# Kernel optimization log

Hardware: AMD Instinct MI355X
Metric: run time of the kernel (lower is better)

## Reference

```python
import jax, jax.numpy as jnp
import numpy as np

N_NODES = 100000
N_EDGES = 1600000
HIDDEN = 64
NUM_GRAPHS = 512


def setup_inputs() -> dict:
    key = jax.random.key(0)
    k1, k2, k3, k4, k5, k6 = jax.random.split(key, 6)
    x = jax.random.normal(k1, (N_NODES, HIDDEN), dtype=jnp.float32)
    edge_index = jax.random.randint(k2, (2, N_EDGES), 0, N_NODES, dtype=jnp.int64)
    batch = jnp.sort(jax.random.randint(k3, (N_NODES,), 0, NUM_GRAPHS, dtype=jnp.int64))
    # SAGPooling's internal GraphConv(64 -> 1): lin_rel (with bias) on aggregated
    # neighbor features, lin_root (no bias) on self features.
    s = 1.0 / np.sqrt(HIDDEN)
    W_rel = jax.random.uniform(k4, (HIDDEN, 1), dtype=jnp.float32, minval=-s, maxval=s)
    b_rel = jax.random.uniform(k5, (1,), dtype=jnp.float32, minval=-s, maxval=s)
    W_root = jax.random.uniform(k6, (HIDDEN, 1), dtype=jnp.float32, minval=-s, maxval=s)
    return {"x": x, "edge_index": edge_index, "batch": batch,
            "W_rel": W_rel, "b_rel": b_rel, "W_root": W_root}


def reference(x, edge_index, batch, W_rel, b_rel, W_root):
    n = x.shape[0]
    src, dst = edge_index[0], edge_index[1]
    # GraphConv (aggr='add'): sum x_j over in-edges, then lin_rel(aggr)+lin_root(x)
    aggr = jax.ops.segment_sum(x[src], dst, num_segments=n)          # [N, H]
    score = (aggr @ W_rel + b_rel + x @ W_root)[:, 0]                # [N]
    # min_score=-1 -> scores softmax-normalized per graph; all nodes kept in order
    m = jax.ops.segment_max(score, batch, num_segments=NUM_GRAPHS)   # [G]
    e = jnp.exp(score - m[batch])
    z = jax.ops.segment_sum(e, batch, num_segments=NUM_GRAPHS)       # [G]
    att = e / z[batch]                                               # [N]
    att_x = x * att[:, None]                                         # [N, H]
    # global_add_pool
    return jax.ops.segment_sum(att_x, batch, num_segments=NUM_GRAPHS)  # [G, H]
```

## Files before the change

### kernel.cpp

```cpp
#include <hip/hip_runtime.h>
#include <math.h>
#include <stdint.h>


#define H 64
#define TILE 4096
#define NTHR_S 1024
#define EPT (TILE / NTHR_S)
#define BUCKET_SZ 256
#define MAX_NB 400
#define NREP 8
#define SUBCAP 768
#define CAP (NREP * SUBCAP)
#define PSCALE 16384.0f
#define INV_PSCALE 6.103515625e-05f

__global__ __launch_bounds__(256) void node_prep(
    const float4* __restrict__ x4, const float4* __restrict__ W_rel4,
    const float4* __restrict__ W_root4,
    float* __restrict__ p, float* __restrict__ r,
    float* __restrict__ num, float* __restrict__ z,
    unsigned int* __restrict__ cursor,
    int n_nodes, int num_elems, int n_graphs, int nb)
{
    int gid = (int)(blockIdx.x * blockDim.x + threadIdx.x);
    if (gid < num_elems) num[gid] = 0.0f;
    else if (gid < num_elems + n_graphs) z[gid - num_elems] = 0.0f;
    else if (gid < num_elems + n_graphs + nb * NREP) {
        int idx = gid - num_elems - n_graphs;
        int rep = idx / nb;
        int k   = idx - rep * nb;
        cursor[idx] = (unsigned int)(k * CAP + rep * SUBCAP);
    }

    int node = blockIdx.x * 64 + (threadIdx.x >> 2);
    int q    = threadIdx.x & 3;
    if (node >= n_nodes) return;

    float pv = 0.0f, rv = 0.0f;
    #pragma unroll
    for (int kk = 0; kk < 4; ++kk) {
        float4 v  = x4[node * 16 + kk * 4 + q];
        float4 wr = W_rel4[kk * 4 + q];
        float4 wo = W_root4[kk * 4 + q];
        pv += v.x * wr.x + v.y * wr.y + v.z * wr.z + v.w * wr.w;
        rv += v.x * wo.x + v.y * wo.y + v.z * wo.z + v.w * wo.w;
    }
    pv += __shfl_xor(pv, 1, 64); pv += __shfl_xor(pv, 2, 64);
    rv += __shfl_xor(rv, 1, 64); rv += __shfl_xor(rv, 2, 64);
    if (q == 0) { p[node] = pv; r[node] = rv; }
}

__global__ __launch_bounds__(NTHR_S) void edge_sort(
    const int* __restrict__ src, const int* __restrict__ dst,
    const float* __restrict__ p,
    unsigned int* __restrict__ cursor, unsigned int* __restrict__ sorted_g,
    int n_edges, int nb)
{
    __shared__ unsigned int hist[MAX_NB];
    __shared__ unsigned int offs[MAX_NB];
    __shared__ unsigned int gbase[MAX_NB];
    __shared__ unsigned int wtot[8];
    __shared__ unsigned int svals[TILE];
    __shared__ unsigned short sbid[TILE];

    int b = blockIdx.x;
    int rep = b & (NREP - 1);
    int base = b * TILE;
    int tile_n = min(TILE, n_edges - base);
    int tid = threadIdx.x;

    if (tid < nb) hist[tid] = 0;
    __syncthreads();

    unsigned int dd[EPT]; int ss[EPT];
    float pv[EPT];
    unsigned int bk[EPT], pk[EPT], slot[EPT];

    int j0 = tid * EPT;
    if (j0 + EPT <= tile_n) {
        int4 s4 = *(const int4*)(src + base + j0);
        int4 d4 = *(const int4*)(dst + base + j0);
        ss[0] = s4.x; ss[1] = s4.y; ss[2] = s4.z; ss[3] = s4.w;
        dd[0] = (unsigned int)d4.x; dd[1] = (unsigned int)d4.y;
        dd[2] = (unsigned int)d4.z; dd[3] = (unsigned int)d4.w;
    } else {
        #pragma unroll
        for (int u = 0; u < EPT; ++u) {
            int j = j0 + u;
            if (j < tile_n) { ss[u] = src[base + j];
                              dd[u] = (unsigned int)dst[base + j]; }
            else dd[u] = 0xFFFFFFFFu;
        }
    }
    #pragma unroll
    for (int u = 0; u < EPT; ++u)
        if (dd[u] != 0xFFFFFFFFu) pv[u] = p[ss[u]];
    #pragma unroll
    for (int u = 0; u < EPT; ++u) {
        if (dd[u] != 0xFFFFFFFFu) {
            bk[u] = dd[u] >> 8;
            int q = (int)__float2int_rn(pv[u] * PSCALE);
            q = max(-8388607, min(8388607, q));
            pk[u] = ((unsigned int)q << 8) | (dd[u] & 255u);
            slot[u] = atomicAdd(&hist[bk[u]], 1u);
        }
    }
    __syncthreads();

    int wv = tid >> 6, ln = tid & 63;
    unsigned int v = 0, xs = 0;
    if (wv < 7) {
        int bin = wv * 64 + ln;
        v = (bin < nb) ? hist[bin] : 0;
        xs = v;
        #pragma unroll
        for (int off = 1; off < 64; off <<= 1) {
            unsigned int y = __shfl_up(xs, off, 64);
            if (ln >= off) xs += y;
        }
        if (ln == 63) wtot[wv] = xs;
    }
    __syncthreads();
    if (wv < 7) {
        int bin = wv * 64 + ln;
        unsigned int pre = 0;
        #pragma unroll
        for (int w2 = 0; w2 < 7; ++w2)
            pre += (w2 < wv) ? wtot[w2] : 0u;
        if (bin < nb) {
            offs[bin]  = pre + xs - v;
            gbase[bin] = v ? atomicAdd(&cursor[rep * nb + bin], v) : 0u;
        }
    }
    __syncthreads();

    #pragma unroll
    for (int u = 0; u < EPT; ++u) {
        if (dd[u] != 0xFFFFFFFFu) {
            unsigned int pos = offs[bk[u]] + slot[u];
            svals[pos] = pk[u];
            sbid[pos]  = (unsigned short)bk[u];
        }
    }
    __syncthreads();

    for (int j = tid; j < tile_n; j += NTHR_S) {
        unsigned int bb = sbid[j];
        unsigned int gi = gbase[bb] + ((unsigned int)j - offs[bb]);
        unsigned int lim = bb * (unsigned int)CAP
                         + (unsigned int)(rep + 1) * SUBCAP;
        if (gi < lim)
            sorted_g[gi] = svals[j];
    }
}

__global__ __launch_bounds__(512) void bucket_pool(
    const unsigned int* __restrict__ sorted_g,
    const unsigned int* __restrict__ cursor,
    const float* __restrict__ r,
    const float* __restrict__ x,
    const int* __restrict__ batch,
    float* __restrict__ num, float* __restrict__ z,
    int n_nodes, int nb)
{
    __shared__ int acc[BUCKET_SZ];
    __shared__ float e_lds[BUCKET_SZ];
    __shared__ int g_lds[BUCKET_SZ];
    __shared__ unsigned int cnts[NREP];
    __shared__ float pnum[2 * NREP][H];
    __shared__ float pz[2 * NREP];
    __shared__ int   sgid[2 * NREP];

    int k = blockIdx.x;
    int tid = threadIdx.x;
    int node0 = k * BUCKET_SZ;

    if (tid < BUCKET_SZ) acc[tid] = 0;
    else {
        int t2 = tid - BUCKET_SZ;
        int node = node0 + t2;
        g_lds[t2] = (node < n_nodes) ? batch[node] : -1;
    }
    if (tid < NREP) {
        unsigned int begr = (unsigned int)(k * CAP + tid * SUBCAP);
        cnts[tid] = min(cursor[tid * nb + k] - begr, (unsigned int)SUBCAP);
    }
    if (tid < 2 * NREP) sgid[tid] = -1;
    __syncthreads();

    {
        int wv = tid >> 6, ln = tid & 63;
        unsigned int beg = (unsigned int)(k * CAP + wv * SUBCAP);
        unsigned int cnt = cnts[wv];
        unsigned int n4  = cnt & ~3u;
        for (unsigned int j = ln * 4; j < n4; j += 256) {
            uint4 v = *(const uint4*)(sorted_g + beg + j);
            atomicAdd(&acc[v.x & 255u], (int)v.x >> 8);
            atomicAdd(&acc[v.y & 255u], (int)v.y >> 8);
            atomicAdd(&acc[v.z & 255u], (int)v.z >> 8);
            atomicAdd(&acc[v.w & 255u], (int)v.w >> 8);
        }
        for (unsigned int j = n4 + ln; j < cnt; j += 64) {
            unsigned int v = sorted_g[beg + j];
            atomicAdd(&acc[v & 255u], (int)v >> 8);
        }
    }
    __syncthreads();

    if (tid < BUCKET_SZ) {
        int node = node0 + tid;
        e_lds[tid] = (node < n_nodes)
                   ? __expf((float)acc[tid] * INV_PSCALE + r[node]) : 0.0f;
    }
    __syncthreads();

    int wid = tid >> 6, lane = tid & 63;
    int l0 = wid * 32;
    int row0 = node0 + l0;
    int s0 = wid * 2;
    if (row0 < n_nodes) {
        int rend = min(row0 + 32, n_nodes);
        int gF = g_lds[l0];
        int gL = g_lds[rend - 1 - node0];
        float sA = 0.0f, sB = 0.0f, zA = 0.0f, zB = 0.0f;

        if (rend - row0 == 32) {
            float xv[32];
            const float* xp = x + (size_t)row0 * H + lane;
            #pragma unroll
            for (int u = 0; u < 32; ++u)
                xv[u] = xp[u * H];
            #pragma unroll
            for (int u = 0; u < 32; ++u) {
                int li = l0 + u;
                int g = g_lds[li];
                float e = e_lds[li];
                float v = xv[u] * e;
                if (g == gF)      { sA += v; zA += e; }
                else if (g == gL) { sB += v; zB += e; }
                else {
                    unsafeAtomicAdd(&num[g * H + lane], v);
                    if (lane == 0) unsafeAtomicAdd(&z[g], e);
                }
            }
        } else {
            for (int i = row0; i < rend; ++i) {
                int li = i - node0;
                int g = g_lds[li];
                float e = e_lds[li];
                float v = x[(size_t)i * H + lane] * e;
                if (g == gF)      { sA += v; zA += e; }
                else if (g == gL) { sB += v; zB += e; }
                else {
                    unsafeAtomicAdd(&num[g * H + lane], v);
                    if (lane == 0) unsafeAtomicAdd(&z[g], e);
                }
            }
        }
        pnum[s0][lane] = sA;
        if (lane == 0) { sgid[s0] = gF; pz[s0] = zA; }
        if (gL != gF) {
            pnum[s0 + 1][lane] = sB;
            if (lane == 0) { sgid[s0 + 1] = gL; pz[s0 + 1] = zB; }
        }
    }
    __syncthreads();

    if (wid == 0) {
        float run = 0.0f, runz = 0.0f; int cur = -1;
        for (int s = 0; s < 2 * NREP; ++s) {
            int id = sgid[s];
            if (id < 0) continue;
            float v  = pnum[s][lane];
            float zv = pz[s];
            if (id != cur) {
                if (cur >= 0) {
                    unsafeAtomicAdd(&num[cur * H + lane], run);
                    if (lane == 0) unsafeAtomicAdd(&z[cur], runz);
                }
                cur = id; run = v; runz = zv;
            } else { run += v; runz += zv; }
        }
        if (cur >= 0) {
            unsafeAtomicAdd(&num[cur * H + lane], run);
            if (lane == 0) unsafeAtomicAdd(&z[cur], runz);
        }
    }
}

__global__ __launch_bounds__(256) void finalize(
    const float* __restrict__ num, const float* __restrict__ z,
    float* __restrict__ out, int num_elems)
{
    int i = (int)(blockIdx.x * blockDim.x + threadIdx.x);
    if (i >= num_elems) return;
    float zz = z[i >> 6];
    out[i] = (zz != 0.0f) ? num[i] / zz : 0.0f;
}

extern "C" void kernel_launch(void* const* d_in, const int* in_sizes, int n_in,
                              void* d_out, int out_size, void* d_ws, size_t ws_size,
                              hipStream_t stream)
{
    const float* x      = (const float*)d_in[0];
    const int*   eidx   = (const int*)d_in[1];
    const int*   batch  = (const int*)d_in[2];
    const float* W_rel  = (const float*)d_in[3];
    const float* W_root = (const float*)d_in[5];
    float* out = (float*)d_out;

    const int n_nodes  = in_sizes[0] / H;
    const int n_edges  = in_sizes[1] / 2;
    const int n_graphs = out_size / H;
    const int nb     = (n_nodes + BUCKET_SZ - 1) / BUCKET_SZ;
    const int ntiles = (n_edges + TILE - 1) / TILE;

    const int* src = eidx;
    const int* dst = eidx + n_edges;

    float* p     = (float*)d_ws;
    float* r     = p + n_nodes;
    float* z     = r + n_nodes;
    float* num   = z + n_graphs;
    unsigned int* cursor = (unsigned int*)(num + out_size);
    uintptr_t raw = (uintptr_t)(cursor + nb * NREP);
    unsigned int* sorted_g = (unsigned int*)((raw + 15) & ~(uintptr_t)15);

    int np_blocks = (n_nodes + 63) / 64;
    node_prep<<<np_blocks, 256, 0, stream>>>(
        (const float4*)x, (const float4*)W_rel, (const float4*)W_root,
        p, r, num, z, cursor, n_nodes, out_size, n_graphs, nb);
    edge_sort<<<ntiles, NTHR_S, 0, stream>>>(src, dst, p, cursor, sorted_g,
                                             n_edges, nb);
    bucket_pool<<<nb, 512, 0, stream>>>(sorted_g, cursor, r, x, batch,
                                        num, z, n_nodes, nb);
    finalize<<<(out_size + 255) / 256, 256, 0, stream>>>(num, z, out, out_size);
}
```

Before: 110.5 us.

## Fuse four kernels into one persistent cooperative kernel with grid syncs

Replaces the node_prep, edge_sort, bucket_pool and finalize launches with a single cooperative kernel of 256 blocks of 1024 threads, using grid.sync between phases. Each phase grid-strides over its work (nodes, edge tiles, buckets), which removes three kernel launch gaps. The bucket phase is reshaped for 1024 threads: two waves per replica, 16 rows per wave and 32 segments. The cost is grid-wide barriers, lower occupancy from the large LDS footprint and fixed block count, and ~391 edge tiles over 256 blocks causing load imbalance.

```diff
diff --git a/kernel.cpp b/kernel.cpp
--- a/kernel.cpp
+++ b/kernel.cpp
@@ -1,12 +1,13 @@
 #include <hip/hip_runtime.h>
+#include <hip/hip_cooperative_groups.h>
 #include <math.h>
 #include <stdint.h>
 
+namespace cg = cooperative_groups;
+
 
 #define H 64
 #define TILE 4096
-#define NTHR_S 1024
-#define EPT (TILE / NTHR_S)
 #define BUCKET_SZ 256
 #define MAX_NB 400
 #define NREP 8
@@ -14,289 +15,284 @@
 #define CAP (NREP * SUBCAP)
 #define PSCALE 16384.0f
 #define INV_PSCALE 6.103515625e-05f
-
-__global__ __launch_bounds__(256) void node_prep(
+#define NBLK 256
+#define NTHR 1024
+#define EPT (TILE / NTHR)
+#define NSEG 32
+
+__global__ __launch_bounds__(NTHR) void fused_pipeline(
     const float4* __restrict__ x4, const float4* __restrict__ W_rel4,
     const float4* __restrict__ W_root4,
+    const int* __restrict__ src, const int* __restrict__ dst,
+    const int* __restrict__ batch,
     float* __restrict__ p, float* __restrict__ r,
-    float* __restrict__ num, float* __restrict__ z,
-    unsigned int* __restrict__ cursor,
-    int n_nodes, int num_elems, int n_graphs, int nb)
+    float* __restrict__ z, float* __restrict__ num,
+    unsigned int* __restrict__ cursor, unsigned int* __restrict__ sorted_g,
+    float* __restrict__ out,
+    int n_nodes, int n_edges, int n_graphs, int nb, int ntiles, int out_size)
 {
-    int gid = (int)(blockIdx.x * blockDim.x + threadIdx.x);
-    if (gid < num_elems) num[gid] = 0.0f;
-    else if (gid < num_elems + n_graphs) z[gid - num_elems] = 0.0f;
-    else if (gid < num_elems + n_graphs + nb * NREP) {
-        int idx = gid - num_elems - n_graphs;
-        int rep = idx / nb;
-        int k   = idx - rep * nb;
-        cursor[idx] = (unsigned int)(k * CAP + rep * SUBCAP);
-    }
-
-    int node = blockIdx.x * 64 + (threadIdx.x >> 2);
-    int q    = threadIdx.x & 3;
-    if (node >= n_nodes) return;
-
-    float pv = 0.0f, rv = 0.0f;
-    #pragma unroll
-    for (int kk = 0; kk < 4; ++kk) {
-        float4 v  = x4[node * 16 + kk * 4 + q];
-        float4 wr = W_rel4[kk * 4 + q];
-        float4 wo = W_root4[kk * 4 + q];
-        pv += v.x * wr.x + v.y * wr.y + v.z * wr.z + v.w * wr.w;
-        rv += v.x * wo.x + v.y * wo.y + v.z * wo.z + v.w * wo.w;
-    }
-    pv += __shfl_xor(pv, 1, 64); pv += __shfl_xor(pv, 2, 64);
-    rv += __shfl_xor(rv, 1, 64); rv += __shfl_xor(rv, 2, 64);
-    if (q == 0) { p[node] = pv; r[node] = rv; }
-}
-
-__global__ __launch_bounds__(NTHR_S) void edge_sort(
-    const int* __restrict__ src, const int* __restrict__ dst,
-    const float* __restrict__ p,
-    unsigned int* __restrict__ cursor, unsigned int* __restrict__ sorted_g,
-    int n_edges, int nb)
-{
+    cg::grid_group grid = cg::this_grid();
+
     __shared__ unsigned int hist[MAX_NB];
     __shared__ unsigned int offs[MAX_NB];
     __shared__ unsigned int gbase[MAX_NB];
     __shared__ unsigned int wtot[8];
     __shared__ unsigned int svals[TILE];
     __shared__ unsigned short sbid[TILE];
-
-    int b = blockIdx.x;
-    int rep = b & (NREP - 1);
-    int base = b * TILE;
-    int tile_n = min(TILE, n_edges - base);
-    int tid = threadIdx.x;
-
-    if (tid < nb) hist[tid] = 0;
-    __syncthreads();
-
-    unsigned int dd[EPT]; int ss[EPT];
-    float pv[EPT];
-    unsigned int bk[EPT], pk[EPT], slot[EPT];
-
-    int j0 = tid * EPT;
-    if (j0 + EPT <= tile_n) {
-        int4 s4 = *(const int4*)(src + base + j0);
-        int4 d4 = *(const int4*)(dst + base + j0);
-        ss[0] = s4.x; ss[1] = s4.y; ss[2] = s4.z; ss[3] = s4.w;
-        dd[0] = (unsigned int)d4.x; dd[1] = (unsigned int)d4.y;
-        dd[2] = (unsigned int)d4.z; dd[3] = (unsigned int)d4.w;
-    } else {
-        #pragma unroll
-        for (int u = 0; u < EPT; ++u) {
-            int j = j0 + u;
-            if (j < tile_n) { ss[u] = src[base + j];
-                              dd[u] = (unsigned int)dst[base + j]; }
-            else dd[u] = 0xFFFFFFFFu;
-        }
-    }
-    #pragma unroll
-    for (int u = 0; u < EPT; ++u)
-        if (dd[u] != 0xFFFFFFFFu) pv[u] = p[ss[u]];
-    #pragma unroll
-    for (int u = 0; u < EPT; ++u) {
-        if (dd[u] != 0xFFFFFFFFu) {
-            bk[u] = dd[u] >> 8;
-            int q = (int)__float2int_rn(pv[u] * PSCALE);
-            q = max(-8388607, min(8388607, q));
-            pk[u] = ((unsigned int)q << 8) | (dd[u] & 255u);
-            slot[u] = atomicAdd(&hist[bk[u]], 1u);
-        }
-    }
-    __syncthreads();
-
-    int wv = tid >> 6, ln = tid & 63;
-    unsigned int v = 0, xs = 0;
-    if (wv < 7) {
-        int bin = wv * 64 + ln;
-        v = (bin < nb) ? hist[bin] : 0;
-        xs = v;
-        #pragma unroll
-        for (int off = 1; off < 64; off <<= 1) {
-            unsigned int y = __shfl_up(xs, off, 64);
-            if (ln >= off) xs += y;
-        }
-        if (ln == 63) wtot[wv] = xs;
-    }
-    __syncthreads();
-    if (wv < 7) {
-        int bin = wv * 64 + ln;
-        unsigned int pre = 0;
-        #pragma unroll
-        for (int w2 = 0; w2 < 7; ++w2)
-            pre += (w2 < wv) ? wtot[w2] : 0u;
-        if (bin < nb) {
-            offs[bin]  = pre + xs - v;
-            gbase[bin] = v ? atomicAdd(&cursor[rep * nb + bin], v) : 0u;
-        }
-    }
-    __syncthreads();
-
-    #pragma unroll
-    for (int u = 0; u < EPT; ++u) {
-        if (dd[u] != 0xFFFFFFFFu) {
-            unsigned int pos = offs[bk[u]] + slot[u];
-            svals[pos] = pk[u];
-            sbid[pos]  = (unsigned short)bk[u];
-        }
-    }
-    __syncthreads();
-
-    for (int j = tid; j < tile_n; j += NTHR_S) {
-        unsigned int bb = sbid[j];
-        unsigned int gi = gbase[bb] + ((unsigned int)j - offs[bb]);
-        unsigned int lim = bb * (unsigned int)CAP
-                         + (unsigned int)(rep + 1) * SUBCAP;
-        if (gi < lim)
-            sorted_g[gi] = svals[j];
-    }
-}
-
-__global__ __launch_bounds__(512) void bucket_pool(
-    const unsigned int* __restrict__ sorted_g,
-    const unsigned int* __restrict__ cursor,
-    const float* __restrict__ r,
-    const float* __restrict__ x,
-    const int* __restrict__ batch,
-    float* __restrict__ num, float* __restrict__ z,
-    int n_nodes, int nb)
-{
     __shared__ int acc[BUCKET_SZ];
     __shared__ float e_lds[BUCKET_SZ];
     __shared__ int g_lds[BUCKET_SZ];
     __shared__ unsigned int cnts[NREP];
-    __shared__ float pnum[2 * NREP][H];
-    __shared__ float pz[2 * NREP];
-    __shared__ int   sgid[2 * NREP];
-
-    int k = blockIdx.x;
-    int tid = threadIdx.x;
-    int node0 = k * BUCKET_SZ;
-
-    if (tid < BUCKET_SZ) acc[tid] = 0;
-    else {
-        int t2 = tid - BUCKET_SZ;
-        int node = node0 + t2;
-        g_lds[t2] = (node < n_nodes) ? batch[node] : -1;
-    }
-    if (tid < NREP) {
-        unsigned int begr = (unsigned int)(k * CAP + tid * SUBCAP);
-        cnts[tid] = min(cursor[tid * nb + k] - begr, (unsigned int)SUBCAP);
-    }
-    if (tid < 2 * NREP) sgid[tid] = -1;
-    __syncthreads();
+    __shared__ float pnum[NSEG][H];
+    __shared__ float pz[NSEG];
+    __shared__ int   sgid[NSEG];
+
+    int tid = threadIdx.x, bid = blockIdx.x;
+    int gt  = bid * NTHR + tid;
+    int wid = tid >> 6, lane = tid & 63;
+
+    if (gt < out_size) num[gt] = 0.0f;
+    else if (gt < out_size + n_graphs) z[gt - out_size] = 0.0f;
+    else if (gt < out_size + n_graphs + nb * NREP) {
+        int idx = gt - out_size - n_graphs;
+        int rep = idx / nb;
+        int k   = idx - rep * nb;
+        cursor[idx] = (unsigned int)(k * CAP + rep * SUBCAP);
+    }
 
     {
-        int wv = tid >> 6, ln = tid & 63;
-        unsigned int beg = (unsigned int)(k * CAP + wv * SUBCAP);
-        unsigned int cnt = cnts[wv];
-        unsigned int n4  = cnt & ~3u;
-        for (unsigned int j = ln * 4; j < n4; j += 256) {
-            uint4 v = *(const uint4*)(sorted_g + beg + j);
-            atomicAdd(&acc[v.x & 255u], (int)v.x >> 8);
-            atomicAdd(&acc[v.y & 255u], (int)v.y >> 8);
-            atomicAdd(&acc[v.z & 255u], (int)v.z >> 8);
-            atomicAdd(&acc[v.w & 255u], (int)v.w >> 8);
-        }
-        for (unsigned int j = n4 + ln; j < cnt; j += 64) {
-            unsigned int v = sorted_g[beg + j];
-            atomicAdd(&acc[v & 255u], (int)v >> 8);
-        }
-    }
-    __syncthreads();
-
-    if (tid < BUCKET_SZ) {
-        int node = node0 + tid;
-        e_lds[tid] = (node < n_nodes)
-                   ? __expf((float)acc[tid] * INV_PSCALE + r[node]) : 0.0f;
-    }
-    __syncthreads();
-
-    int wid = tid >> 6, lane = tid & 63;
-    int l0 = wid * 32;
-    int row0 = node0 + l0;
-    int s0 = wid * 2;
-    if (row0 < n_nodes) {
-        int rend = min(row0 + 32, n_nodes);
-        int gF = g_lds[l0];
-        int gL = g_lds[rend - 1 - node0];
-        float sA = 0.0f, sB = 0.0f, zA = 0.0f, zB = 0.0f;
-
-        if (rend - row0 == 32) {
-            float xv[32];
-            const float* xp = x + (size_t)row0 * H + lane;
+        int q = gt & 3;
+        for (int node = (gt >> 2); node < n_nodes; node += (NBLK * NTHR) / 4) {
+            float pv = 0.0f, rv = 0.0f;
             #pragma unroll
-            for (int u = 0; u < 32; ++u)
-                xv[u] = xp[u * H];
+            for (int kk = 0; kk < 4; ++kk) {
+                float4 v  = x4[node * 16 + kk * 4 + q];
+                float4 wr = W_rel4[kk * 4 + q];
+                float4 wo = W_root4[kk * 4 + q];
+                pv += v.x * wr.x + v.y * wr.y + v.z * wr.z + v.w * wr.w;
+                rv += v.x * wo.x + v.y * wo.y + v.z * wo.z + v.w * wo.w;
+            }
+            pv += __shfl_xor(pv, 1, 64); pv += __shfl_xor(pv, 2, 64);
+            rv += __shfl_xor(rv, 1, 64); rv += __shfl_xor(rv, 2, 64);
+            if (q == 0) { p[node] = pv; r[node] = rv; }
+        }
+    }
+    grid.sync();
+
+    for (int t = bid; t < ntiles; t += NBLK) {
+        int rep = t & (NREP - 1);
+        int base = t * TILE;
+        int tile_n = min(TILE, n_edges - base);
+
+        if (tid < nb) hist[tid] = 0;
+        __syncthreads();
+
+        unsigned int dd[EPT]; int ss[EPT];
+        float pv[EPT];
+        unsigned int bk[EPT], pk[EPT], slot[EPT];
+
+        int j0 = tid * EPT;
+        if (j0 + EPT <= tile_n) {
+            int4 s4 = *(const int4*)(src + base + j0);
+            int4 d4 = *(const int4*)(dst + base + j0);
+            ss[0] = s4.x; ss[1] = s4.y; ss[2] = s4.z; ss[3] = s4.w;
+            dd[0] = (unsigned int)d4.x; dd[1] = (unsigned int)d4.y;
+            dd[2] = (unsigned int)d4.z; dd[3] = (unsigned int)d4.w;
+        } else {
             #pragma unroll
-            for (int u = 0; u < 32; ++u) {
-                int li = l0 + u;
-                int g = g_lds[li];
-                float e = e_lds[li];
-                float v = xv[u] * e;
-                if (g == gF)      { sA += v; zA += e; }
-                else if (g == gL) { sB += v; zB += e; }
-                else {
-                    unsafeAtomicAdd(&num[g * H + lane], v);
-                    if (lane == 0) unsafeAtomicAdd(&z[g], e);
+            for (int u = 0; u < EPT; ++u) {
+                int j = j0 + u;
+                if (j < tile_n) { ss[u] = src[base + j];
+                                  dd[u] = (unsigned int)dst[base + j]; }
+                else dd[u] = 0xFFFFFFFFu;
+            }
+        }
+        #pragma unroll
+        for (int u = 0; u < EPT; ++u)
+            if (dd[u] != 0xFFFFFFFFu) pv[u] = p[ss[u]];
+        #pragma unroll
+        for (int u = 0; u < EPT; ++u) {
+            if (dd[u] != 0xFFFFFFFFu) {
+                bk[u] = dd[u] >> 8;
+                int qv = (int)__float2int_rn(pv[u] * PSCALE);
+                qv = max(-8388607, min(8388607, qv));
+                pk[u] = ((unsigned int)qv << 8) | (dd[u] & 255u);
+                slot[u] = atomicAdd(&hist[bk[u]], 1u);
+            }
+        }
+        __syncthreads();
+
+        unsigned int v = 0, xs = 0;
+        if (wid < 7) {
+            int bin = wid * 64 + lane;
+            v = (bin < nb) ? hist[bin] : 0;
+            xs = v;
+            #pragma unroll
+            for (int off = 1; off < 64; off <<= 1) {
+                unsigned int y = __shfl_up(xs, off, 64);
+                if (lane >= off) xs += y;
+            }
+            if (lane == 63) wtot[wid] = xs;
+        }
+        __syncthreads();
+        if (wid < 7) {
+            int bin = wid * 64 + lane;
+            unsigned int pre = 0;
+            #pragma unroll
+            for (int w2 = 0; w2 < 7; ++w2)
+                pre += (w2 < wid) ? wtot[w2] : 0u;
+            if (bin < nb) {
+                offs[bin]  = pre + xs - v;
+                gbase[bin] = v ? atomicAdd(&cursor[rep * nb + bin], v) : 0u;
+            }
+        }
+        __syncthreads();
+
+        #pragma unroll
+        for (int u = 0; u < EPT; ++u) {
+            if (dd[u] != 0xFFFFFFFFu) {
+                unsigned int pos = offs[bk[u]] + slot[u];
+                svals[pos] = pk[u];
+                sbid[pos]  = (unsigned short)bk[u];
+            }
+        }
+        __syncthreads();
+
+        for (int j = tid; j < tile_n; j += NTHR) {
+            unsigned int bb = sbid[j];
+            unsigned int gi = gbase[bb] + ((unsigned int)j - offs[bb]);
+            unsigned int lim = bb * (unsigned int)CAP
+                             + (unsigned int)(rep + 1) * SUBCAP;
+            if (gi < lim)
+                sorted_g[gi] = svals[j];
+        }
+        __syncthreads();
+    }
+    grid.sync();
+
+    const float* x = (const float*)x4;
+    for (int k = bid; k < nb; k += NBLK) {
+        __syncthreads();
+        int node0 = k * BUCKET_SZ;
+
+        if (tid < BUCKET_SZ) acc[tid] = 0;
+        else if (tid < 2 * BUCKET_SZ) {
+            int t2 = tid - BUCKET_SZ;
+            int node = node0 + t2;
+            g_lds[t2] = (node < n_nodes) ? batch[node] : -1;
+        }
+        if (tid < NREP) {
+            unsigned int begr = (unsigned int)(k * CAP + tid * SUBCAP);
+            cnts[tid] = min(cursor[tid * nb + k] - begr, (unsigned int)SUBCAP);
+        }
+        if (tid < NSEG) sgid[tid] = -1;
+        __syncthreads();
+
+        {
+            int rep_id = wid >> 1;
+            int sub    = ((wid & 1) << 6) + lane;
+            unsigned int beg = (unsigned int)(k * CAP + rep_id * SUBCAP);
+            unsigned int cnt = cnts[rep_id];
+            unsigned int n4  = cnt & ~3u;
+            for (unsigned int j = (unsigned int)sub * 4; j < n4; j += 512) {
+                uint4 vv = *(const uint4*)(sorted_g + beg + j);
+                atomicAdd(&acc[vv.x & 255u], (int)vv.x >> 8);
+                atomicAdd(&acc[vv.y & 255u], (int)vv.y >> 8);
+                atomicAdd(&acc[vv.z & 255u], (int)vv.z >> 8);
+                atomicAdd(&acc[vv.w & 255u], (int)vv.w >> 8);
+            }
+            for (unsigned int j = n4 + (unsigned int)sub; j < cnt; j += 128) {
+                unsigned int vv = sorted_g[beg + j];
+                atomicAdd(&acc[vv & 255u], (int)vv >> 8);
+            }
+        }
+        __syncthreads();
+
+        if (tid < BUCKET_SZ) {
+            int node = node0 + tid;
+            e_lds[tid] = (node < n_nodes)
+                       ? __expf((float)acc[tid] * INV_PSCALE + r[node]) : 0.0f;
+        }
+        __syncthreads();
+
+        int l0 = wid * 16;
+        int row0 = node0 + l0;
+        int s0 = wid * 2;
+        if (row0 < n_nodes) {
+            int rend = min(row0 + 16, n_nodes);
+            int gF = g_lds[l0];
+            int gL = g_lds[rend - 1 - node0];
+            float sA = 0.0f, sB = 0.0f, zA = 0.0f, zB = 0.0f;
+
+            if (rend - row0 == 16) {
+                float xv[16];
+                const float* xp = x + (size_t)row0 * H + lane;
+                #pragma unroll
+                for (int u = 0; u < 16; ++u)
+                    xv[u] = xp[u * H];
+                #pragma unroll
+                for (int u = 0; u < 16; ++u) {
+                    int li = l0 + u;
+                    int g = g_lds[li];
+                    float e = e_lds[li];
+                    float vv = xv[u] * e;
+                    if (g == gF)      { sA += vv; zA += e; }
+                    else if (g == gL) { sB += vv; zB += e; }
+                    else {
+                        unsafeAtomicAdd(&num[g * H + lane], vv);
+                        if (lane == 0) unsafeAtomicAdd(&z[g], e);
+                    }
                 }
-            }
-        } else {
-            for (int i = row0; i < rend; ++i) {
-                int li = i - node0;
-                int g = g_lds[li];
-                float e = e_lds[li];
-                float v = x[(size_t)i * H + lane] * e;
-                if (g == gF)      { sA += v; zA += e; }
-                else if (g == gL) { sB += v; zB += e; }
-                else {
-                    unsafeAtomicAdd(&num[g * H + lane], v);
-                    if (lane == 0) unsafeAtomicAdd(&z[g], e);
+            } else {
+                for (int i = row0; i < rend; ++i) {
+                    int li = i - node0;
+                    int g = g_lds[li];
+                    float e = e_lds[li];
+                    float vv = x[(size_t)i * H + lane] * e;
+                    if (g == gF)      { sA += vv; zA += e; }
+                    else if (g == gL) { sB += vv; zB += e; }
+                    else {
+                        unsafeAtomicAdd(&num[g * H + lane], vv);
+                        if (lane == 0) unsafeAtomicAdd(&z[g], e);
+                    }
                 }
             }
-        }
-        pnum[s0][lane] = sA;
-        if (lane == 0) { sgid[s0] = gF; pz[s0] = zA; }
-        if (gL != gF) {
-            pnum[s0 + 1][lane] = sB;
-            if (lane == 0) { sgid[s0 + 1] = gL; pz[s0 + 1] = zB; }
-        }
-    }
-    __syncthreads();
-
-    if (wid == 0) {
-        float run = 0.0f, runz = 0.0f; int cur = -1;
-        for (int s = 0; s < 2 * NREP; ++s) {
-            int id = sgid[s];
-            if (id < 0) continue;
-            float v  = pnum[s][lane];
-            float zv = pz[s];
-            if (id != cur) {
-                if (cur >= 0) {
-                    unsafeAtomicAdd(&num[cur * H + lane], run);
-                    if (lane == 0) unsafeAtomicAdd(&z[cur], runz);
-                }
-                cur = id; run = v; runz = zv;
-            } else { run += v; runz += zv; }
-        }
-        if (cur >= 0) {
-            unsafeAtomicAdd(&num[cur * H + lane], run);
-            if (lane == 0) unsafeAtomicAdd(&z[cur], runz);
-        }
-    }
-}
-
-__global__ __launch_bounds__(256) void finalize(
-    const float* __restrict__ num, const float* __restrict__ z,
-    float* __restrict__ out, int num_elems)
-{
-    int i = (int)(blockIdx.x * blockDim.x + threadIdx.x);
-    if (i >= num_elems) return;
-    float zz = z[i >> 6];
-    out[i] = (zz != 0.0f) ? num[i] / zz : 0.0f;
+            pnum[s0][lane] = sA;
+            if (lane == 0) { sgid[s0] = gF; pz[s0] = zA; }
+            if (gL != gF) {
+                pnum[s0 + 1][lane] = sB;
+                if (lane == 0) { sgid[s0 + 1] = gL; pz[s0 + 1] = zB; }
+            }
+        }
+        __syncthreads();
+
+        if (wid == 0) {
+            float run = 0.0f, runz = 0.0f; int cur = -1;
+            for (int s = 0; s < NSEG; ++s) {
+                int id = sgid[s];
+                if (id < 0) continue;
+                float vv = pnum[s][lane];
+                float zv = pz[s];
+                if (id != cur) {
+                    if (cur >= 0) {
+                        unsafeAtomicAdd(&num[cur * H + lane], run);
+                        if (lane == 0) unsafeAtomicAdd(&z[cur], runz);
+                    }
+                    cur = id; run = vv; runz = zv;
+                } else { run += vv; runz += zv; }
+            }
+            if (cur >= 0) {
+                unsafeAtomicAdd(&num[cur * H + lane], run);
+                if (lane == 0) unsafeAtomicAdd(&z[cur], runz);
+            }
+        }
+    }
+    grid.sync();
+
+    if (gt < out_size) {
+        float zz = z[gt >> 6];
+        out[gt] = (zz != 0.0f) ? num[gt] / zz : 0.0f;
+    }
 }
 
 extern "C" void kernel_launch(void* const* d_in, const int* in_sizes, int n_in,
@@ -327,13 +323,20 @@
     uintptr_t raw = (uintptr_t)(cursor + nb * NREP);
     unsigned int* sorted_g = (unsigned int*)((raw + 15) & ~(uintptr_t)15);
 
-    int np_blocks = (n_nodes + 63) / 64;
-    node_prep<<<np_blocks, 256, 0, stream>>>(
-        (const float4*)x, (const float4*)W_rel, (const float4*)W_root,
-        p, r, num, z, cursor, n_nodes, out_size, n_graphs, nb);
-    edge_sort<<<ntiles, NTHR_S, 0, stream>>>(src, dst, p, cursor, sorted_g,
-                                             n_edges, nb);
-    bucket_pool<<<nb, 512, 0, stream>>>(sorted_g, cursor, r, x, batch,
-                                        num, z, n_nodes, nb);
-    finalize<<<(out_size + 255) / 256, 256, 0, stream>>>(num, z, out, out_size);
+    const float4* x4  = (const float4*)x;
+    const float4* wr4 = (const float4*)W_rel;
+    const float4* wo4 = (const float4*)W_root;
+    int nn = n_nodes, ne = n_edges, ng = n_graphs, nbv = nb, nt = ntiles,
+        os = out_size;
+
+    void* args[] = {
+        (void*)&x4, (void*)&wr4, (void*)&wo4,
+        (void*)&src, (void*)&dst, (void*)&batch,
+        (void*)&p, (void*)&r, (void*)&z, (void*)&num,
+        (void*)&cursor, (void*)&sorted_g, (void*)&out,
+        (void*)&nn, (void*)&ne, (void*)&ng, (void*)&nbv, (void*)&nt,
+        (void*)&os
+    };
+    hipLaunchCooperativeKernel((const void*)fused_pipeline,
+                               dim3(NBLK), dim3(NTHR), args, 0, stream);
 }
```

Result: slower. 217.5 us (+96.9%).
